# Performance work log

Hardware: AMD Instinct MI355X
Metric: run time of the kernel (lower is better)

Reference implementation:

```python
import jax, jax.numpy as jnp
import numpy as np

B, N, D, H = 1024, 32, 512, 4
HD = D // H


def setup_inputs() -> dict:
    key = jax.random.key(0)
    k1, k2, k3 = jax.random.split(key, 3)
    scale = 1.0 / np.sqrt(D)  # keep logits in a sane range (mimics xavier init)
    return {
        "agent_hiddens": jax.random.normal(k1, (B, N, D), dtype=jnp.float32),
        "padding_mask": jnp.zeros((B, N), dtype=bool),
        "in_proj_weight": jax.random.normal(k2, (3 * D, D), dtype=jnp.float32) * scale,
        "in_proj_bias": jnp.zeros((3 * D,), dtype=jnp.float32),
        "out_proj_weight": jax.random.normal(k3, (D, D), dtype=jnp.float32) * scale,
        "out_proj_bias": jnp.zeros((D,), dtype=jnp.float32),
    }


def reference(agent_hiddens, padding_mask, in_proj_weight, in_proj_bias,
              out_proj_weight, out_proj_bias):
    # Equivalent to the per-agent loop: full self-attention over the N agents
    # with the diagonal (self) and padded agents masked out of the keys.
    qkv = agent_hiddens @ in_proj_weight.T + in_proj_bias      # (B, N, 3D)
    q, k, v = jnp.split(qkv, 3, axis=-1)
    # (B, H, N, HD)
    q = q.reshape(B, N, H, HD).transpose(0, 2, 1, 3)
    k = k.reshape(B, N, H, HD).transpose(0, 2, 1, 3)
    v = v.reshape(B, N, H, HD).transpose(0, 2, 1, 3)

    scores = jnp.einsum('bhqd,bhkd->bhqk', q, k) / jnp.sqrt(jnp.float32(HD))
    self_mask = jnp.eye(N, dtype=bool)                         # exclude j == i
    mask = self_mask[None, None, :, :] | padding_mask[:, None, None, :]
    scores = jnp.where(mask, -jnp.inf, scores)
    attn = jax.nn.softmax(scores, axis=-1)                     # (B, H, N, N)

    ctx = jnp.einsum('bhqk,bhkd->bhqd', attn, v)               # (B, H, N, HD)
    ctx = ctx.transpose(0, 2, 1, 3).reshape(B, N, D)
    return ctx @ out_proj_weight.T + out_proj_bias
```

## Files before the change

kernel.cpp:

```cpp
#include <hip/hip_runtime.h>
#include <hip/hip_bf16.h>


typedef __attribute__((ext_vector_type(4)))  float f32x4;
typedef __attribute__((ext_vector_type(16))) float f32x16;
typedef __attribute__((ext_vector_type(8)))  short bf16x8;
typedef __attribute__((ext_vector_type(4)))  short bf16x4;
typedef __attribute__((ext_vector_type(4)))  int   i32x4;

__device__ __forceinline__ unsigned short f2bf(float f) {
    unsigned u = __builtin_bit_cast(unsigned, f);
    u = (u + 0x7FFFu + ((u >> 16) & 1u)) >> 16;
    return (unsigned short)u;
}

__device__ __forceinline__ void gload_lds16(const void* g, void* l) {
    __builtin_amdgcn_global_load_lds(
        (const __attribute__((address_space(1))) void*)g,
        (__attribute__((address_space(3))) void*)l, 16, 0, 0);
}

__global__ __launch_bounds__(256)
void cvt3_kernel(const float* __restrict__ s0, unsigned short* __restrict__ d0, int n0,
                 const float* __restrict__ s1, unsigned short* __restrict__ d1, int n1,
                 const float* __restrict__ s2, unsigned short* __restrict__ d2, int n2)
{
    int i = blockIdx.x * 256 + threadIdx.x;
    const float* s; unsigned short* d; int k;
    if (i < n0)                { s = s0; d = d0; k = i; }
    else if (i < n0 + n1)      { s = s1; d = d1; k = i - n0; }
    else if (i < n0 + n1 + n2) { s = s2; d = d2; k = i - n0 - n1; }
    else return;
    f32x4 v = ((const f32x4*)s)[k];
    bf16x4 o;
#pragma unroll
    for (int e = 0; e < 4; ++e) o[e] = (short)f2bf(v[e]);
    ((bf16x4*)d)[k] = o;
}

template<int MODE>
__global__ __launch_bounds__(256)
void gemm_bt(const unsigned short* __restrict__ A, const unsigned short* __restrict__ Bw,
             const float* __restrict__ bias, void* __restrict__ Cout, int ldc, int ntx)
{
    __shared__ unsigned short As[2][128 * 64];
    __shared__ unsigned short Bs[2][128 * 64];

    const int t = threadIdx.x;
    const int nwg = gridDim.x;
    const int cpx = nwg >> 3;
    const int lin = blockIdx.x;
    const int swz = (lin & 7) * cpx + (lin >> 3);
    const int bx = swz % ntx, by = swz / ntx;
    const int mbase = by * 128, nbase = bx * 128;

    const int w = t >> 6, l = t & 63;
    const int wr = w >> 1, wc = w & 1;
    const int lg = l >> 4, lr = l & 15;

    int soff[4];
#pragma unroll
    for (int i = 0; i < 4; ++i) {
        int p = i * 256 + t;
        int row = p >> 3, pc = p & 7;
        soff[i] = row * 512 + (pc ^ (row & 7)) * 8;
    }
    const unsigned short* Ab = A  + (size_t)mbase * 512;
    const unsigned short* Bb = Bw + (size_t)nbase * 512;

    f32x4 acc[4][4] = {};

    auto STAGE = [&](int buf, int ks) {
#pragma unroll
        for (int i = 0; i < 4; ++i) {
            gload_lds16(Ab + soff[i] + ks, &As[buf][(i * 256 + w * 64) * 8]);
            gload_lds16(Bb + soff[i] + ks, &Bs[buf][(i * 256 + w * 64) * 8]);
        }
    };
    auto COMPUTE = [&](int buf) {
#pragma unroll
        for (int kk = 0; kk < 64; kk += 32) {
            const int lc = (kk >> 3) + lg;
            bf16x8 af[4], bfr[4];
#pragma unroll
            for (int mi = 0; mi < 4; ++mi) {
                int r = wr * 64 + mi * 16 + lr;
                af[mi] = *(const bf16x8*)&As[buf][r * 64 + ((lc ^ (r & 7)) << 3)];
            }
#pragma unroll
            for (int ni = 0; ni < 4; ++ni) {
                int n = wc * 64 + ni * 16 + lr;
                bfr[ni] = *(const bf16x8*)&Bs[buf][n * 64 + ((lc ^ (n & 7)) << 3)];
            }
#pragma unroll
            for (int mi = 0; mi < 4; ++mi)
#pragma unroll
                for (int ni = 0; ni < 4; ++ni)
                    acc[mi][ni] = __builtin_amdgcn_mfma_f32_16x16x32_bf16(
                        af[mi], bfr[ni], acc[mi][ni], 0, 0, 0);
        }
    };

    int cur = 0;
    STAGE(0, 0);
    __syncthreads();
#pragma unroll 1
    for (int ti = 0; ti < 7; ++ti) {
        STAGE(cur ^ 1, (ti + 1) << 6);
        COMPUTE(cur);
        __syncthreads();
        cur ^= 1;
    }
    COMPUTE(cur);

    float brow[4][4];
    if (MODE == 2) {
#pragma unroll
        for (int mi = 0; mi < 4; ++mi)
#pragma unroll
            for (int ri = 0; ri < 4; ++ri)
                brow[mi][ri] = bias[mbase + wr * 64 + mi * 16 + lg * 4 + ri];
    }
#pragma unroll
    for (int ni = 0; ni < 4; ++ni) {
        int col = nbase + wc * 64 + ni * 16 + lr;
        float bcol = (MODE == 2) ? 0.f : bias[col];
#pragma unroll
        for (int mi = 0; mi < 4; ++mi) {
            int row0 = mbase + wr * 64 + mi * 16 + lg * 4;
#pragma unroll
            for (int ri = 0; ri < 4; ++ri) {
                float v = acc[mi][ni][ri] + ((MODE == 2) ? brow[mi][ri] : bcol);
                if (MODE == 1)
                    ((float*)Cout)[(size_t)(row0 + ri) * ldc + col] = v;
                else
                    ((unsigned short*)Cout)[(size_t)(row0 + ri) * ldc + col] = f2bf(v);
            }
        }
    }
}

__global__ __launch_bounds__(256)
void attn_mfma(const unsigned short* __restrict__ qk,
               const unsigned short* __restrict__ Vt,
               const unsigned char* __restrict__ pad,
               unsigned short* __restrict__ ctx)
{
    const int wid = blockIdx.x * 4 + (threadIdx.x >> 6);
    const int b = wid >> 2, h = wid & 3;
    const int l = threadIdx.x & 63;
    const int q = l & 31;
    const int hi = l >> 5;

    const unsigned short* rowp = qk + (size_t)(b * 32 + q) * 1024 + h * 128;

    f32x16 s = {};
#pragma unroll
    for (int st = 0; st < 8; ++st) {
        int d0 = st * 16 + hi * 8;
        bf16x8 kf = *(const bf16x8*)(rowp + 512 + d0);
        bf16x8 qf = *(const bf16x8*)(rowp + d0);
        s = __builtin_amdgcn_mfma_f32_32x32x16_bf16(kf, qf, s, 0, 0, 0);
    }

    unsigned long long bal = __ballot(pad[b * 32 + q] != 0);
    unsigned padbits = (unsigned)bal | (unsigned)(bal >> 32);
    const float sc = 0.08838834764831845f;
    float sv[16];
    float m = -INFINITY;
#pragma unroll
    for (int r = 0; r < 16; ++r) {
        int k = (r & 3) + 8 * (r >> 2) + 4 * hi;
        bool msk = (k == q) || ((padbits >> k) & 1u);
        sv[r] = msk ? -INFINITY : s[r] * sc;
        m = fmaxf(m, sv[r]);
    }
    m = fmaxf(m, __shfl_xor(m, 32));
    float p[16], sum = 0.f;
#pragma unroll
    for (int r = 0; r < 16; ++r) { p[r] = __expf(sv[r] - m); sum += p[r]; }
    sum += __shfl_xor(sum, 32);
    const float inv = 1.0f / sum;
#pragma unroll
    for (int r = 0; r < 16; ++r) p[r] *= inv;

    bf16x8 pa[2];
#pragma unroll
    for (int t2 = 0; t2 < 2; ++t2) {
        unsigned pk[4], pw[4];
#pragma unroll
        for (int i = 0; i < 4; ++i)
            pk[i] = ((unsigned)f2bf(p[8 * t2 + 2 * i + 1]) << 16)
                  |  (unsigned)f2bf(p[8 * t2 + 2 * i]);
#pragma unroll
        for (int i = 0; i < 4; ++i)
            pw[i] = (unsigned)__shfl_xor((int)pk[i], 32);
        unsigned w0 = hi ? pw[2] : pk[0];
        unsigned w1 = hi ? pw[3] : pk[1];
        unsigned w2 = hi ? pk[2] : pw[0];
        unsigned w3 = hi ? pk[3] : pw[1];
        i32x4 wv = {(int)w0, (int)w1, (int)w2, (int)w3};
        pa[t2] = __builtin_bit_cast(bf16x8, wv);
    }

#pragma unroll
    for (int dt = 0; dt < 4; ++dt) {
        f32x16 c = {};
#pragma unroll
        for (int t2 = 0; t2 < 2; ++t2) {
            const unsigned short* vp =
                Vt + (size_t)(h * 128 + dt * 32 + q) * 32768 + b * 32 + t2 * 16 + hi * 8;
            bf16x8 vb = *(const bf16x8*)vp;
            c = __builtin_amdgcn_mfma_f32_32x32x16_bf16(pa[t2], vb, c, 0, 0, 0);
        }
        unsigned short* co = ctx + (size_t)(b * 32) * 512 + h * 128 + dt * 32 + q;
#pragma unroll
        for (int r = 0; r < 16; ++r) {
            int qr = (r & 3) + 8 * (r >> 2) + 4 * hi;
            co[(size_t)qr * 512] = f2bf(c[r]);
        }
    }
}

extern "C" void kernel_launch(void* const* d_in, const int* in_sizes, int n_in,
                              void* d_out, int out_size, void* d_ws, size_t ws_size,
                              hipStream_t stream)
{
    const float*         X    = (const float*)d_in[0];
    const unsigned char* pad  = (const unsigned char*)d_in[1];
    const float*         Win  = (const float*)d_in[2];
    const float*         bin  = (const float*)d_in[3];
    const float*         Wout = (const float*)d_in[4];
    const float*         bout = (const float*)d_in[5];
    float*               out  = (float*)d_out;

    char* ws = (char*)d_ws;
    unsigned short* qkb   = (unsigned short*)(ws);
    unsigned short* Vtb   = (unsigned short*)(ws + (size_t)67108864);
    unsigned short* Xb    = (unsigned short*)(ws + (size_t)100663296);
    unsigned short* ctxb  = Xb;
    unsigned short* Winb  = (unsigned short*)(ws + (size_t)134217728);
    unsigned short* Woutb = (unsigned short*)(ws + (size_t)135790592);

    dim3 blk(256);
    cvt3_kernel<<<dim3(17408), blk, 0, stream>>>(X, Xb, 4194304,
                                                 Win, Winb, 196608,
                                                 Wout, Woutb, 65536);
    gemm_bt<0><<<dim3(2048), blk, 0, stream>>>(Xb, Winb, bin, qkb, 1024, 8);
    gemm_bt<2><<<dim3(1024), blk, 0, stream>>>(Winb + (size_t)1024 * 512, Xb,
                                               bin + 1024, Vtb, 32768, 256);
    attn_mfma<<<dim3(1024), blk, 0, stream>>>(qkb, Vtb, pad, ctxb);
    gemm_bt<1><<<dim3(1024), blk, 0, stream>>>(ctxb, Woutb, bout, out, 512, 4);
}
```

Baseline: 257.7 us.

## Merge QK and V projection GEMMs and store per-batch-head contiguous layouts

The separate Q/K and V^T projection launches become a single 3072-block kernel that picks its role from the block index. Q, K and V^T are written in per-(batch, head) contiguous tiles, so each attention block reads compact regions instead of strided rows. This removes one launch and fills the GPU better across the two GEMMs, and the attention loads become more local. The cost is scattered 2-byte epilogue stores in the GEMM, which may coalesce poorly.

Result: faster. 252.6 us (-2.0%).

```diff
diff --git a/kernel.cpp b/kernel.cpp
--- a/kernel.cpp
+++ b/kernel.cpp
@@ -38,21 +38,33 @@
     ((bf16x4*)d)[k] = o;
 }
 
-template<int MODE>
 __global__ __launch_bounds__(256)
-void gemm_bt(const unsigned short* __restrict__ A, const unsigned short* __restrict__ Bw,
-             const float* __restrict__ bias, void* __restrict__ Cout, int ldc, int ntx)
+void gemm_qkvt(const unsigned short* __restrict__ Xb,
+               const unsigned short* __restrict__ Winb,
+               const float* __restrict__ bin,
+               unsigned short* __restrict__ qkb2,
+               unsigned short* __restrict__ vtb2)
 {
     __shared__ unsigned short As[2][128 * 64];
     __shared__ unsigned short Bs[2][128 * 64];
 
     const int t = threadIdx.x;
-    const int nwg = gridDim.x;
-    const int cpx = nwg >> 3;
     const int lin = blockIdx.x;
-    const int swz = (lin & 7) * cpx + (lin >> 3);
-    const int bx = swz % ntx, by = swz / ntx;
-    const int mbase = by * 128, nbase = bx * 128;
+    const bool isVt = lin >= 2048;
+    int mbase, nbase;
+    const unsigned short *Ap, *Bp;
+    if (!isVt) {
+        int swz = (lin & 7) * 256 + (lin >> 3);
+        nbase = (swz & 7) * 128;
+        mbase = (swz >> 3) * 128;
+        Ap = Xb; Bp = Winb;
+    } else {
+        int l2 = lin - 2048;
+        int swz = (l2 & 7) * 128 + (l2 >> 3);
+        nbase = (swz & 255) * 128;
+        mbase = (swz >> 8) * 128;
+        Ap = Winb + (size_t)1024 * 512; Bp = Xb;
+    }
 
     const int w = t >> 6, l = t & 63;
     const int wr = w >> 1, wc = w & 1;
@@ -65,8 +77,8 @@
         int row = p >> 3, pc = p & 7;
         soff[i] = row * 512 + (pc ^ (row & 7)) * 8;
     }
-    const unsigned short* Ab = A  + (size_t)mbase * 512;
-    const unsigned short* Bb = Bw + (size_t)nbase * 512;
+    const unsigned short* Ab = Ap + (size_t)mbase * 512;
+    const unsigned short* Bb = Bp + (size_t)nbase * 512;
 
     f32x4 acc[4][4] = {};
 
@@ -113,53 +125,156 @@
     }
     COMPUTE(cur);
 
-    float brow[4][4];
-    if (MODE == 2) {
-#pragma unroll
-        for (int mi = 0; mi < 4; ++mi)
-#pragma unroll
-            for (int ri = 0; ri < 4; ++ri)
-                brow[mi][ri] = bias[mbase + wr * 64 + mi * 16 + lg * 4 + ri];
-    }
+    if (!isVt) {
+#pragma unroll
+        for (int ni = 0; ni < 4; ++ni) {
+            int col = nbase + wc * 64 + ni * 16 + lr;
+            float bcol = bin[col];
+            int sel = col >> 9;
+            int h   = (col >> 7) & 3;
+            int d   = col & 127;
+            unsigned short* ob = qkb2 + (size_t)h * 8192 + (size_t)sel * 4096 + d;
+#pragma unroll
+            for (int mi = 0; mi < 4; ++mi) {
+                int row0 = mbase + wr * 64 + mi * 16 + lg * 4;
+#pragma unroll
+                for (int ri = 0; ri < 4; ++ri) {
+                    int row = row0 + ri;
+                    int bb = row >> 5, ag = row & 31;
+                    ob[(size_t)bb * 32768 + ag * 128] = f2bf(acc[mi][ni][ri] + bcol);
+                }
+            }
+        }
+    } else {
+#pragma unroll
+        for (int ni = 0; ni < 4; ++ni) {
+            int col = nbase + wc * 64 + ni * 16 + lr;
+            int bb = col >> 5, ag = col & 31;
+            unsigned short* ob = vtb2 + (size_t)bb * 16384 + ag;
+#pragma unroll
+            for (int mi = 0; mi < 4; ++mi) {
+                int row0 = mbase + wr * 64 + mi * 16 + lg * 4;
+#pragma unroll
+                for (int ri = 0; ri < 4; ++ri) {
+                    int row = row0 + ri;
+                    float v = acc[mi][ni][ri] + bin[1024 + row];
+                    int h = row >> 7, d = row & 127;
+                    ob[(size_t)h * 4096 + d * 32] = f2bf(v);
+                }
+            }
+        }
+    }
+}
+
+__global__ __launch_bounds__(256)
+void gemm_out(const unsigned short* __restrict__ A, const unsigned short* __restrict__ Bw,
+              const float* __restrict__ bias, float* __restrict__ Cout, int ldc, int ntx)
+{
+    __shared__ unsigned short As[2][128 * 64];
+    __shared__ unsigned short Bs[2][128 * 64];
+
+    const int t = threadIdx.x;
+    const int nwg = gridDim.x;
+    const int cpx = nwg >> 3;
+    const int lin = blockIdx.x;
+    const int swz = (lin & 7) * cpx + (lin >> 3);
+    const int bx = swz % ntx, by = swz / ntx;
+    const int mbase = by * 128, nbase = bx * 128;
+
+    const int w = t >> 6, l = t & 63;
+    const int wr = w >> 1, wc = w & 1;
+    const int lg = l >> 4, lr = l & 15;
+
+    int soff[4];
+#pragma unroll
+    for (int i = 0; i < 4; ++i) {
+        int p = i * 256 + t;
+        int row = p >> 3, pc = p & 7;
+        soff[i] = row * 512 + (pc ^ (row & 7)) * 8;
+    }
+    const unsigned short* Ab = A  + (size_t)mbase * 512;
+    const unsigned short* Bb = Bw + (size_t)nbase * 512;
+
+    f32x4 acc[4][4] = {};
+
+    auto STAGE = [&](int buf, int ks) {
+#pragma unroll
+        for (int i = 0; i < 4; ++i) {
+            gload_lds16(Ab + soff[i] + ks, &As[buf][(i * 256 + w * 64) * 8]);
+            gload_lds16(Bb + soff[i] + ks, &Bs[buf][(i * 256 + w * 64) * 8]);
+        }
+    };
+    auto COMPUTE = [&](int buf) {
+#pragma unroll
+        for (int kk = 0; kk < 64; kk += 32) {
+            const int lc = (kk >> 3) + lg;
+            bf16x8 af[4], bfr[4];
+#pragma unroll
+            for (int mi = 0; mi < 4; ++mi) {
+                int r = wr * 64 + mi * 16 + lr;
+                af[mi] = *(const bf16x8*)&As[buf][r * 64 + ((lc ^ (r & 7)) << 3)];
+            }
+#pragma unroll
+            for (int ni = 0; ni < 4; ++ni) {
+                int n = wc * 64 + ni * 16 + lr;
+                bfr[ni] = *(const bf16x8*)&Bs[buf][n * 64 + ((lc ^ (n & 7)) << 3)];
+            }
+#pragma unroll
+            for (int mi = 0; mi < 4; ++mi)
+#pragma unroll
+                for (int ni = 0; ni < 4; ++ni)
+                    acc[mi][ni] = __builtin_amdgcn_mfma_f32_16x16x32_bf16(
+                        af[mi], bfr[ni], acc[mi][ni], 0, 0, 0);
+        }
+    };
+
+    int cur = 0;
+    STAGE(0, 0);
+    __syncthreads();
+#pragma unroll 1
+    for (int ti = 0; ti < 7; ++ti) {
+        STAGE(cur ^ 1, (ti + 1) << 6);
+        COMPUTE(cur);
+        __syncthreads();
+        cur ^= 1;
+    }
+    COMPUTE(cur);
+
 #pragma unroll
     for (int ni = 0; ni < 4; ++ni) {
         int col = nbase + wc * 64 + ni * 16 + lr;
-        float bcol = (MODE == 2) ? 0.f : bias[col];
+        float bcol = bias[col];
 #pragma unroll
         for (int mi = 0; mi < 4; ++mi) {
             int row0 = mbase + wr * 64 + mi * 16 + lg * 4;
 #pragma unroll
-            for (int ri = 0; ri < 4; ++ri) {
-                float v = acc[mi][ni][ri] + ((MODE == 2) ? brow[mi][ri] : bcol);
-                if (MODE == 1)
-                    ((float*)Cout)[(size_t)(row0 + ri) * ldc + col] = v;
-                else
-                    ((unsigned short*)Cout)[(size_t)(row0 + ri) * ldc + col] = f2bf(v);
-            }
+            for (int ri = 0; ri < 4; ++ri)
+                Cout[(size_t)(row0 + ri) * ldc + col] = acc[mi][ni][ri] + bcol;
         }
     }
 }
 
 __global__ __launch_bounds__(256)
-void attn_mfma(const unsigned short* __restrict__ qk,
-               const unsigned short* __restrict__ Vt,
+void attn_mfma(const unsigned short* __restrict__ qkb2,
+               const unsigned short* __restrict__ vtb2,
                const unsigned char* __restrict__ pad,
                unsigned short* __restrict__ ctx)
 {
-    const int wid = blockIdx.x * 4 + (threadIdx.x >> 6);
-    const int b = wid >> 2, h = wid & 3;
+    const int b = blockIdx.x;
+    const int h = threadIdx.x >> 6;
     const int l = threadIdx.x & 63;
     const int q = l & 31;
     const int hi = l >> 5;
 
-    const unsigned short* rowp = qk + (size_t)(b * 32 + q) * 1024 + h * 128;
+    const unsigned short* qb = qkb2 + (size_t)b * 32768 + (size_t)h * 8192;
+    const unsigned short* kb = qb + 4096;
 
     f32x16 s = {};
 #pragma unroll
     for (int st = 0; st < 8; ++st) {
         int d0 = st * 16 + hi * 8;
-        bf16x8 kf = *(const bf16x8*)(rowp + 512 + d0);
-        bf16x8 qf = *(const bf16x8*)(rowp + d0);
+        bf16x8 kf = *(const bf16x8*)(kb + q * 128 + d0);
+        bf16x8 qf = *(const bf16x8*)(qb + q * 128 + d0);
         s = __builtin_amdgcn_mfma_f32_32x32x16_bf16(kf, qf, s, 0, 0, 0);
     }
 
@@ -203,14 +318,13 @@
         pa[t2] = __builtin_bit_cast(bf16x8, wv);
     }
 
+    const unsigned short* vb_ = vtb2 + (size_t)b * 16384 + (size_t)h * 4096;
 #pragma unroll
     for (int dt = 0; dt < 4; ++dt) {
         f32x16 c = {};
 #pragma unroll
         for (int t2 = 0; t2 < 2; ++t2) {
-            const unsigned short* vp =
-                Vt + (size_t)(h * 128 + dt * 32 + q) * 32768 + b * 32 + t2 * 16 + hi * 8;
-            bf16x8 vb = *(const bf16x8*)vp;
+            bf16x8 vb = *(const bf16x8*)(vb_ + (dt * 32 + q) * 32 + t2 * 16 + hi * 8);
             c = __builtin_amdgcn_mfma_f32_32x32x16_bf16(pa[t2], vb, c, 0, 0, 0);
         }
         unsigned short* co = ctx + (size_t)(b * 32) * 512 + h * 128 + dt * 32 + q;
@@ -235,8 +349,8 @@
     float*               out  = (float*)d_out;
 
     char* ws = (char*)d_ws;
-    unsigned short* qkb   = (unsigned short*)(ws);
-    unsigned short* Vtb   = (unsigned short*)(ws + (size_t)67108864);
+    unsigned short* qkb2  = (unsigned short*)(ws);
+    unsigned short* vtb2  = (unsigned short*)(ws + (size_t)67108864);
     unsigned short* Xb    = (unsigned short*)(ws + (size_t)100663296);
     unsigned short* ctxb  = Xb;
     unsigned short* Winb  = (unsigned short*)(ws + (size_t)134217728);
@@ -246,9 +360,7 @@
     cvt3_kernel<<<dim3(17408), blk, 0, stream>>>(X, Xb, 4194304,
                                                  Win, Winb, 196608,
                                                  Wout, Woutb, 65536);
-    gemm_bt<0><<<dim3(2048), blk, 0, stream>>>(Xb, Winb, bin, qkb, 1024, 8);
-    gemm_bt<2><<<dim3(1024), blk, 0, stream>>>(Winb + (size_t)1024 * 512, Xb,
-                                               bin + 1024, Vtb, 32768, 256);
-    attn_mfma<<<dim3(1024), blk, 0, stream>>>(qkb, Vtb, pad, ctxb);
-    gemm_bt<1><<<dim3(1024), blk, 0, stream>>>(ctxb, Woutb, bout, out, 512, 4);
-}
+    gemm_qkvt<<<dim3(3072), blk, 0, stream>>>(Xb, Winb, bin, qkb2, vtb2);
+    attn_mfma<<<dim3(1024), blk, 0, stream>>>(qkb2, vtb2, pad, ctxb);
+    gemm_out<<<dim3(1024), blk, 0, stream>>>(ctxb, Woutb, bout, out, 512, 4);
+}
```
